# Kernel tuning notes

Hardware: AMD Instinct MI355X
Metric: run time of the kernel (lower is better)

The kernel has to match this reference:

```python
import jax, jax.numpy as jnp
import numpy as np

K = 20          # neighbors per point (knn includes the point itself, as in PyG knn)
EPS = 1e-5      # BatchNorm eps (eval mode, running stats)


def _lrelu(x):
    return jax.nn.leaky_relu(x, 0.2)


def _bn(x, g, beta, mu, var):
    # eval-mode BatchNorm1d over last (feature) axis
    return (x - mu) * (g * jax.lax.rsqrt(var + EPS)) + beta


def _edge_conv(x, W, g, beta, mu, var):
    # x: [B, N, F]. Dynamic kNN graph per batch element, edge feature [x_i, x_j - x_i],
    # Linear(no bias) -> BN -> LeakyReLU(0.2), max-aggregate over neighbors.
    sq = jnp.sum(x * x, axis=-1)                                   # [B, N]
    d2 = sq[:, :, None] + sq[:, None, :] - 2.0 * jnp.einsum('bnf,bmf->bnm', x, x)
    _, idx = jax.lax.top_k(-d2, K)                                 # [B, N, K] (self is nearest)
    xj = jax.vmap(lambda xb, ib: xb[ib])(x, idx)                   # [B, N, K, F]
    xi = jnp.broadcast_to(x[:, :, None, :], xj.shape)
    e = jnp.concatenate([xi, xj - xi], axis=-1) @ W                # [B, N, K, out]
    return jnp.max(_lrelu(_bn(e, g, beta, mu, var)), axis=2)       # [B, N, out]


def setup_inputs() -> dict:
    key = jax.random.key(0)
    ks = iter(jax.random.split(key, 64))
    B, N = 8, 2048
    d = {"pos": jax.random.normal(next(ks), (B, N, 3), jnp.float32)}

    def bn_params(name, dim):
        d["g" + name] = 0.5 + jax.random.uniform(next(ks), (dim,), jnp.float32)
        d["beta" + name] = 0.1 * jax.random.normal(next(ks), (dim,), jnp.float32)
        d["mu" + name] = 0.1 * jax.random.normal(next(ks), (dim,), jnp.float32)
        d["var" + name] = 0.5 + jax.random.uniform(next(ks), (dim,), jnp.float32)

    def lin(name, din, dout):
        d["W" + name] = jax.random.normal(next(ks), (din, dout), jnp.float32) / np.sqrt(din).astype(np.float32)

    lin("1", 2 * 3, 64);    bn_params("1", 64)
    lin("2", 2 * 64, 64);   bn_params("2", 64)
    lin("3", 2 * 64, 128);  bn_params("3", 128)
    lin("4", 2 * 128, 256); bn_params("4", 256)
    lin("m", 512, 1024);    bn_params("m", 1024)
    lin("a", 2048, 512);    bn_params("a", 512)
    lin("b", 512, 256);     bn_params("b", 256)
    d["bias_b"] = 0.01 * jax.random.normal(next(ks), (256,), jnp.float32)
    lin("c", 256, 40)
    d["bias_c"] = 0.01 * jax.random.normal(next(ks), (40,), jnp.float32)
    return d


def reference(pos, W1, g1, beta1, mu1, var1, W2, g2, beta2, mu2, var2,
              W3, g3, beta3, mu3, var3, W4, g4, beta4, mu4, var4,
              Wm, gm, betam, mum, varm, Wa, ga, betaa, mua, vara,
              Wb, gb, betab, mub, varb, bias_b, Wc, bias_c):
    x1 = _edge_conv(pos, W1, g1, beta1, mu1, var1)   # [B, N, 64]
    x2 = _edge_conv(x1, W2, g2, beta2, mu2, var2)    # [B, N, 64]
    x3 = _edge_conv(x2, W3, g3, beta3, mu3, var3)    # [B, N, 128]
    x4 = _edge_conv(x3, W4, g4, beta4, mu4, var4)    # [B, N, 256]
    h = jnp.concatenate([x1, x2, x3, x4], axis=-1)   # [B, N, 512]
    h = _lrelu(_bn(h @ Wm, gm, betam, mum, varm))    # [B, N, 1024]
    pooled = jnp.concatenate([jnp.max(h, axis=1), jnp.mean(h, axis=1)], axis=-1)  # [B, 2048]
    h = _lrelu(_bn(pooled @ Wa, ga, betaa, mua, vara))            # [B, 512]
    h = _lrelu(_bn(h @ Wb + bias_b, gb, betab, mub, varb))        # [B, 256]
    return h @ Wc + bias_c                                        # [B, 40]
```

## Files before the change

### kernel.cpp

```cpp
#include <hip/hip_runtime.h>
#include <cstdint>
#include <cstddef>

#define NPTS 2048
#define BATCH 8
#define KNN 20
#define BIGF 3.402823466e38f

typedef short bf16x8 __attribute__((ext_vector_type(8)));
typedef float f32x4 __attribute__((ext_vector_type(4)));

__device__ __forceinline__ unsigned short f2bf(float v) {
    uint32_t u = __float_as_uint(v);
    uint32_t r = (u + 0x7FFFu + ((u >> 16) & 1u)) >> 16;
    return (unsigned short)r;
}
__device__ __forceinline__ float bf2f(unsigned short h) {
    return __uint_as_float(((uint32_t)h) << 16);
}
__device__ __forceinline__ uint32_t flipkey(float d) {
    uint32_t u = __float_as_uint(d);
    return (u & 0x80000000u) ? ~u : (u | 0x80000000u);
}
__device__ __forceinline__ uint32_t d2key(float acc, float si, float sj) {
    return flipkey(fmaf(-2.f, acc, si + sj));
}
__device__ __forceinline__ uint64_t shfl_xor_u64(uint64_t v, int m) {
    int lo = __shfl_xor((int)(uint32_t)v, m, 64);
    int hi = __shfl_xor((int)(uint32_t)(v >> 32), m, 64);
    return ((uint64_t)(uint32_t)hi << 32) | (uint32_t)lo;
}

__global__ __launch_bounds__(256) void sq_kernel(const float* __restrict__ x, int lda, int F,
                                                 float* __restrict__ sq)
{
    int p = blockIdx.x * 256 + threadIdx.x;
    const float* xp = x + (size_t)p * lda;
    float s = 0.f;
    for (int f = 0; f < F; ++f) { float v = xp[f]; s = fmaf(v, v, s); }
    sq[p] = s;
}

__global__ __launch_bounds__(256) void distk_kernel(const float* __restrict__ x, int lda,
                                                    const float* __restrict__ sq,
                                                    unsigned short* __restrict__ d2u16,
                                                    int F, int b0)
{
    __shared__ __align__(16) float As[8][132];
    __shared__ __align__(16) float Bs[8][132];
    const int b  = b0 + blockIdx.z;
    const int i0 = blockIdx.x * 128;
    const int j0 = blockIdx.y * 128;
    const float* xb  = x + (size_t)b * NPTS * lda;
    const float* sqb = sq + (size_t)b * NPTS;
    const int t  = threadIdx.x;
    const int tx = t & 15, ty = t >> 4;
    const int lrow = t >> 1, lkq = (t & 1) * 4;

    float acc[8][8];
#pragma unroll
    for (int r = 0; r < 8; ++r)
#pragma unroll
        for (int c = 0; c < 8; ++c) acc[r][c] = 0.f;

    for (int k0 = 0; k0 < F; k0 += 8) {
        const float* sa = xb + (size_t)(i0 + lrow) * lda + k0 + lkq;
        const float* sb = xb + (size_t)(j0 + lrow) * lda + k0 + lkq;
        if (k0 + 8 <= F) {
            float4 a4 = *reinterpret_cast<const float4*>(sa);
            float4 b4 = *reinterpret_cast<const float4*>(sb);
            As[lkq + 0][lrow] = a4.x; As[lkq + 1][lrow] = a4.y;
            As[lkq + 2][lrow] = a4.z; As[lkq + 3][lrow] = a4.w;
            Bs[lkq + 0][lrow] = b4.x; Bs[lkq + 1][lrow] = b4.y;
            Bs[lkq + 2][lrow] = b4.z; Bs[lkq + 3][lrow] = b4.w;
        } else {
#pragma unroll
            for (int q = 0; q < 4; ++q) {
                int kk = k0 + lkq + q;
                As[lkq + q][lrow] = (kk < F) ? sa[q] : 0.f;
                Bs[lkq + q][lrow] = (kk < F) ? sb[q] : 0.f;
            }
        }
        __syncthreads();
#pragma unroll
        for (int k = 0; k < 8; ++k) {
            float4 a0 = *reinterpret_cast<const float4*>(&As[k][ty * 4]);
            float4 a1 = *reinterpret_cast<const float4*>(&As[k][64 + ty * 4]);
            float4 c0 = *reinterpret_cast<const float4*>(&Bs[k][tx * 4]);
            float4 c1 = *reinterpret_cast<const float4*>(&Bs[k][64 + tx * 4]);
            float av[8] = {a0.x, a0.y, a0.z, a0.w, a1.x, a1.y, a1.z, a1.w};
            float bv[8] = {c0.x, c0.y, c0.z, c0.w, c1.x, c1.y, c1.z, c1.w};
#pragma unroll
            for (int r = 0; r < 8; ++r)
#pragma unroll
                for (int c = 0; c < 8; ++c) acc[r][c] = fmaf(av[r], bv[c], acc[r][c]);
        }
        __syncthreads();
    }

    unsigned short* db = d2u16 + (size_t)blockIdx.z * NPTS * NPTS;
#pragma unroll
    for (int r = 0; r < 8; ++r) {
        int i = i0 + ((r < 4) ? (ty * 4 + r) : (64 + ty * 4 + r - 4));
        float si = sqb[i];
#pragma unroll
        for (int cq = 0; cq < 2; ++cq) {
            int j = j0 + (cq ? 64 : 0) + tx * 4;
            ushort4 o;
            o.x = (unsigned short)(d2key(acc[r][cq * 4 + 0], si, sqb[j + 0]) >> 16);
            o.y = (unsigned short)(d2key(acc[r][cq * 4 + 1], si, sqb[j + 1]) >> 16);
            o.z = (unsigned short)(d2key(acc[r][cq * 4 + 2], si, sqb[j + 2]) >> 16);
            o.w = (unsigned short)(d2key(acc[r][cq * 4 + 3], si, sqb[j + 3]) >> 16);
            *reinterpret_cast<ushort4*>(&db[(size_t)i * NPTS + j]) = o;
        }
    }
}

template <int F>
__global__ __launch_bounds__(256) void select_kernel(const unsigned short* __restrict__ d2u16,
                                                     const float* __restrict__ x, int lda,
                                                     const float* __restrict__ sq,
                                                     int* __restrict__ idx, int b0)
{
    const int t    = threadIdx.x;
    const int lane = t & 63;
    const int wid  = t >> 6;
    const int row_id = blockIdx.x * 4 + wid;
    const int bz = row_id >> 11;
    const int i  = row_id & 2047;
    const unsigned short* row = d2u16 + ((size_t)bz * NPTS + i) * NPTS;

    uint32_t cand[32];
#pragma unroll
    for (int s = 0; s < 4; ++s) {
        uint4 kv = *reinterpret_cast<const uint4*>(&row[s * 512 + lane * 8]);
        uint32_t cb = (uint32_t)(s * 512 + lane * 8);
        cand[s * 8 + 0] = ((kv.x & 0xFFFFu) << 16) | (cb + 0);
        cand[s * 8 + 1] = (kv.x & 0xFFFF0000u)      | (cb + 1);
        cand[s * 8 + 2] = ((kv.y & 0xFFFFu) << 16) | (cb + 2);
        cand[s * 8 + 3] = (kv.y & 0xFFFF0000u)      | (cb + 3);
        cand[s * 8 + 4] = ((kv.z & 0xFFFFu) << 16) | (cb + 4);
        cand[s * 8 + 5] = (kv.z & 0xFFFF0000u)      | (cb + 5);
        cand[s * 8 + 6] = ((kv.w & 0xFFFFu) << 16) | (cb + 6);
        cand[s * 8 + 7] = (kv.w & 0xFFFF0000u)      | (cb + 7);
    }

    const uint32_t MAXV = 0xFFFFFFFFu;
    uint32_t t1 = MAXV, t2 = MAXV, t3 = MAXV, t4 = MAXV;
#pragma unroll
    for (int s = 0; s < 32; ++s) {
        uint32_t c = cand[s];
        if (c < t4) {
            if (c < t2) {
                t4 = t3; t3 = t2;
                if (c < t1) { t2 = t1; t1 = c; } else t2 = c;
            } else {
                if (c < t3) { t4 = t3; t3 = c; } else t4 = c;
            }
        }
    }

    uint32_t keep = 0, last = 0;
    for (int it = 0; it < KNN; ++it) {
        uint32_t w = t1;
#pragma unroll
        for (int o = 1; o < 64; o <<= 1)
            w = min(w, (uint32_t)__shfl_xor((int)w, o, 64));
        keep = (lane == it) ? w : keep;
        last = w;
        if (t1 == w) {
            t1 = t2; t2 = t3; t3 = t4; t4 = MAXV;
            if (t1 == MAXV) {
#pragma unroll
                for (int s = 0; s < 32; ++s) {
                    uint32_t c = cand[s];
                    if (c > w && c < t4) {
                        if (c < t2) {
                            t4 = t3; t3 = t2;
                            if (c < t1) { t2 = t1; t1 = c; } else t2 = c;
                        } else {
                            if (c < t3) { t4 = t3; t3 = c; } else t4 = c;
                        }
                    }
                }
            }
        }
    }

    int* out = idx + ((size_t)(b0 + bz) * NPTS + i) * KNN;
    const uint32_t thr16 = last >> 16;

    int cnt = 0;
#pragma unroll
    for (int s = 0; s < 32; ++s) cnt += ((cand[s] >> 16) == thr16) ? 1 : 0;
#pragma unroll
    for (int o = 1; o < 64; o <<= 1) cnt += __shfl_xor(cnt, o, 64);

    unsigned long long bm = __ballot(lane < KNN && (keep >> 16) < thr16);
    const int sel_lt = (int)__popcll(bm);
    const int m = KNN - sel_lt;
    const bool fast = (cnt == m);

    if (lane < KNN && (fast || (keep >> 16) < thr16))
        out[lane] = (int)(keep & 0xFFFFu);
    if (fast) return;

    const float* xb  = x + (size_t)(b0 + bz) * NPTS * lda;
    const float* sqb = sq + (size_t)(b0 + bz) * NPTS;
    const float si = sqb[i];
    const float* xi = xb + (size_t)i * lda;

    uint64_t tc[4]; int ntc = 0; bool ovf = false;
#pragma unroll
    for (int s = 0; s < 32; ++s) {
        if ((cand[s] >> 16) == thr16) {
            if (ntc < 4) {
                int j = (int)(cand[s] & 0xFFFFu);
                const float* xj = xb + (size_t)j * lda;
                float dot = 0.f;
#pragma unroll
                for (int k = 0; k < F; ++k) dot = fmaf(xi[k], xj[k], dot);
                uint32_t fk = d2key(dot, si, sqb[j]);
                tc[ntc++] = ((uint64_t)fk << 32) | (uint32_t)j;
            } else ovf = true;
        }
    }
    if (__ballot(ovf)) {
        uint64_t last_ex = 0;
        for (int q = 0; q < m; ++q) {
            uint64_t lm = ~0ull;
            for (int s = 0; s < 32; ++s) {
                if ((cand[s] >> 16) == thr16) {
                    int j = (int)(cand[s] & 0xFFFFu);
                    const float* xj = xb + (size_t)j * lda;
                    float dot = 0.f;
                    for (int k = 0; k < F; ++k) dot = fmaf(xi[k], xj[k], dot);
                    uint64_t e = ((uint64_t)d2key(dot, si, sqb[j]) << 32) | (uint32_t)j;
                    if (e > last_ex && e < lm) lm = e;
                }
            }
#pragma unroll
            for (int o = 1; o < 64; o <<= 1) {
                uint64_t ov = shfl_xor_u64(lm, o);
                lm = (ov < lm) ? ov : lm;
            }
            if (lane == 0) out[sel_lt + q] = (int)(lm & 0xFFFFu);
            last_ex = lm;
        }
        return;
    }
    uint64_t last_ex = 0;
    for (int q = 0; q < m; ++q) {
        uint64_t lm = ~0ull;
#pragma unroll
        for (int u = 0; u < 4; ++u)
            if (u < ntc && tc[u] > last_ex && tc[u] < lm) lm = tc[u];
#pragma unroll
        for (int o = 1; o < 64; o <<= 1) {
            uint64_t ov = shfl_xor_u64(lm, o);
            lm = (ov < lm) ? ov : lm;
        }
        if (lane == 0) out[sel_lt + q] = (int)(lm & 0xFFFFu);
        last_ex = lm;
    }
}

__global__ __launch_bounds__(256) void gemm64_kernel(const float* __restrict__ A, int lda, int F,
                                                     const float* __restrict__ Wfull, int Fout,
                                                     float* __restrict__ apart,
                                                     float* __restrict__ bpart)
{
    __shared__ float As[16][68];
    __shared__ float Bs[16][65];
    const int i0 = blockIdx.x * 64, j0 = blockIdx.y * 64;
    const int half = blockIdx.z;
    const float* Bw = Wfull + (size_t)(half ? F : 0) * Fout;
    float* C = half ? bpart : apart;
    const int t = threadIdx.x, tx = t & 15, ty = t >> 4;
    float acc[4][4];
#pragma unroll
    for (int r = 0; r < 4; ++r)
#pragma unroll
        for (int c = 0; c < 4; ++c) acc[r][c] = 0.f;
    const int arow = t >> 2, akq = (t & 3) * 4;
    const int bk = t >> 4, bj = (t & 15) * 4;
    for (int k0 = 0; k0 < F; k0 += 16) {
#pragma unroll
        for (int q = 0; q < 4; ++q) {
            int kk = k0 + akq + q;
            As[akq + q][arow] = (kk < F) ? A[(size_t)(i0 + arow) * lda + kk] : 0.f;
        }
        {
            int kk = k0 + bk;
#pragma unroll
            for (int q = 0; q < 4; ++q)
                Bs[bk][bj + q] = (kk < F) ? Bw[(size_t)kk * Fout + j0 + bj + q] : 0.f;
        }
        __syncthreads();
#pragma unroll
        for (int k = 0; k < 16; ++k) {
            float a[4], bb[4];
#pragma unroll
            for (int r = 0; r < 4; ++r) a[r] = As[k][ty * 4 + r];
#pragma unroll
            for (int c = 0; c < 4; ++c) bb[c] = Bs[k][tx * 4 + c];
#pragma unroll
            for (int r = 0; r < 4; ++r)
#pragma unroll
                for (int c = 0; c < 4; ++c) acc[r][c] = fmaf(a[r], bb[c], acc[r][c]);
        }
        __syncthreads();
    }
#pragma unroll
    for (int r = 0; r < 4; ++r)
#pragma unroll
        for (int c = 0; c < 4; ++c)
            C[(size_t)(i0 + ty * 4 + r) * Fout + j0 + tx * 4 + c] = acc[r][c];
}

template <int FOUT>
__global__ __launch_bounds__(256) void aggregate_kernel(const float* __restrict__ apart,
                                                        const float* __restrict__ bpart,
                                                        const int* __restrict__ idx,
                                                        const float* __restrict__ g,
                                                        const float* __restrict__ be,
                                                        const float* __restrict__ mu,
                                                        const float* __restrict__ var,
                                                        float* __restrict__ out)
{
    constexpr int G   = FOUT / 4;
    constexpr int PPB = 256 / G;
    const int t  = threadIdx.x;
    const int pi = t / G;
    const int fi = t % G;
    const int p  = blockIdx.x * PPB + pi;
    const int b  = p >> 11;
    const int* nb = idx + (size_t)p * KNN;
    const float4* bp4 = reinterpret_cast<const float4*>(bpart);
    const float4* bb  = bp4 + ((size_t)b << 11) * G;

    float4 m = {-BIGF, -BIGF, -BIGF, -BIGF};
#pragma unroll 4
    for (int k = 0; k < KNN; ++k) {
        int j = nb[k];
        float4 v = bb[(size_t)j * G + fi];
        m.x = fmaxf(m.x, v.x); m.y = fmaxf(m.y, v.y);
        m.z = fmaxf(m.z, v.z); m.w = fmaxf(m.w, v.w);
    }
    float4 av = reinterpret_cast<const float4*>(apart)[(size_t)p * G + fi];
    float4 bv = bp4[(size_t)p * G + fi];
    float4 gg = reinterpret_cast<const float4*>(g)[fi];
    float4 bee = reinterpret_cast<const float4*>(be)[fi];
    float4 muu = reinterpret_cast<const float4*>(mu)[fi];
    float4 vaa = reinterpret_cast<const float4*>(var)[fi];

    float4 r;
    {
        float s, sh, vv, y;
        s = gg.x * rsqrtf(vaa.x + 1e-5f); sh = bee.x - muu.x * s;
        vv = av.x - bv.x + m.x; y = vv * s + sh; r.x = (y >= 0.f) ? y : 0.2f * y;
        s = gg.y * rsqrtf(vaa.y + 1e-5f); sh = bee.y - muu.y * s;
        vv = av.y - bv.y + m.y; y = vv * s + sh; r.y = (y >= 0.f) ? y : 0.2f * y;
        s = gg.z * rsqrtf(vaa.z + 1e-5f); sh = bee.z - muu.z * s;
        vv = av.z - bv.z + m.z; y = vv * s + sh; r.z = (y >= 0.f) ? y : 0.2f * y;
        s = gg.w * rsqrtf(vaa.w + 1e-5f); sh = bee.w - muu.w * s;
        vv = av.w - bv.w + m.w; y = vv * s + sh; r.w = (y >= 0.f) ? y : 0.2f * y;
    }
    *reinterpret_cast<float4*>(out + (size_t)p * 512 + fi * 4) = r;
}

__global__ __launch_bounds__(256) void cvt_kernel(const float* __restrict__ in,
                                                  unsigned short* __restrict__ hi,
                                                  unsigned short* __restrict__ lo)
{
    int i = blockIdx.x * 256 + threadIdx.x;
    const float4* p = reinterpret_cast<const float4*>(in) + (size_t)i * 2;
    float4 a = p[0], b = p[1];
    float v[8] = {a.x, a.y, a.z, a.w, b.x, b.y, b.z, b.w};
    uint32_t h[8], l[8];
#pragma unroll
    for (int q = 0; q < 8; ++q) {
        unsigned short hb = f2bf(v[q]);
        h[q] = hb;
        l[q] = f2bf(v[q] - bf2f(hb));
    }
    uint4 uh, ul;
    uh.x = h[0] | (h[1] << 16); uh.y = h[2] | (h[3] << 16);
    uh.z = h[4] | (h[5] << 16); uh.w = h[6] | (h[7] << 16);
    ul.x = l[0] | (l[1] << 16); ul.y = l[2] | (l[3] << 16);
    ul.z = l[4] | (l[5] << 16); ul.w = l[6] | (l[7] << 16);
    reinterpret_cast<uint4*>(hi)[i] = uh;
    reinterpret_cast<uint4*>(lo)[i] = ul;
}

__global__ __launch_bounds__(256) void cvtT_kernel(const float* __restrict__ Wm,
                                                   unsigned short* __restrict__ hiT,
                                                   unsigned short* __restrict__ loT)
{
    __shared__ float tile[32][33];
    const int n0 = blockIdx.x * 32;
    const int k0 = blockIdx.y * 32;
    const int t = threadIdx.x;
    const int c = t & 31, r = t >> 5;
#pragma unroll
    for (int rr = 0; rr < 4; ++rr)
        tile[r + rr * 8][c] = Wm[(size_t)(k0 + r + rr * 8) * 1024 + n0 + c];
    __syncthreads();
#pragma unroll
    for (int rr = 0; rr < 4; ++rr) {
        int nn = r + rr * 8, kk = c;
        float v = tile[kk][nn];
        unsigned short hb = f2bf(v);
        hiT[(size_t)(n0 + nn) * 512 + k0 + kk] = hb;
        loT[(size_t)(n0 + nn) * 512 + k0 + kk] = f2bf(v - bf2f(hb));
    }
}

__global__ __launch_bounds__(256) void wm_mfma_pool(const unsigned short* __restrict__ AH,
                                                    const unsigned short* __restrict__ AL,
                                                    const unsigned short* __restrict__ BH,
                                                    const unsigned short* __restrict__ BL,
                                                    const float* __restrict__ g,
                                                    const float* __restrict__ be,
                                                    const float* __restrict__ mu,
                                                    const float* __restrict__ var,
                                                    float* __restrict__ partmax,
                                                    float* __restrict__ partsum)
{
    __shared__ unsigned short AsH[128][40], AsL[128][40], BsH[128][40], BsL[128][40];
    __shared__ float redm[4][64], reds[4][64];
    const int t = threadIdx.x;
    const int i0 = blockIdx.x * 128, j0 = blockIdx.y * 128;
    const int lane = t & 63, wid = t >> 6, wy = wid >> 1, wx = wid & 1;
    const int lc = lane & 15, kg = lane >> 4;

    f32x4 acc[4][4];
#pragma unroll
    for (int mi = 0; mi < 4; ++mi)
#pragma unroll
        for (int ni = 0; ni < 4; ++ni) acc[mi][ni] = (f32x4){0.f, 0.f, 0.f, 0.f};

    for (int k0 = 0; k0 < 512; k0 += 32) {
        __syncthreads();
#pragma unroll
        for (int q = 0; q < 2; ++q) {
            int c = t + q * 256;
            int row = c >> 2, ko = (c & 3) * 8;
            *reinterpret_cast<uint4*>(&AsH[row][ko]) =
                *reinterpret_cast<const uint4*>(&AH[(size_t)(i0 + row) * 512 + k0 + ko]);
            *reinterpret_cast<uint4*>(&AsL[row][ko]) =
                *reinterpret_cast<const uint4*>(&AL[(size_t)(i0 + row) * 512 + k0 + ko]);
            *reinterpret_cast<uint4*>(&BsH[row][ko]) =
                *reinterpret_cast<const uint4*>(&BH[(size_t)(j0 + row) * 512 + k0 + ko]);
            *reinterpret_cast<uint4*>(&BsL[row][ko]) =
                *reinterpret_cast<const uint4*>(&BL[(size_t)(j0 + row) * 512 + k0 + ko]);
        }
        __syncthreads();

        bf16x8 aH[4], aL[4], bH[4], bL[4];
#pragma unroll
        for (int mi = 0; mi < 4; ++mi) {
            int ar = wy * 64 + mi * 16 + lc;
            aH[mi] = *reinterpret_cast<const bf16x8*>(&AsH[ar][kg * 8]);
            aL[mi] = *reinterpret_cast<const bf16x8*>(&AsL[ar][kg * 8]);
        }
#pragma unroll
        for (int ni = 0; ni < 4; ++ni) {
            int br = wx * 64 + ni * 16 + lc;
            bH[ni] = *reinterpret_cast<const bf16x8*>(&BsH[br][kg * 8]);
            bL[ni] = *reinterpret_cast<const bf16x8*>(&BsL[br][kg * 8]);
        }
#pragma unroll
        for (int mi = 0; mi < 4; ++mi)
#pragma unroll
            for (int ni = 0; ni < 4; ++ni) {
                acc[mi][ni] = __builtin_amdgcn_mfma_f32_16x16x32_bf16(aH[mi], bH[ni], acc[mi][ni], 0, 0, 0);
                acc[mi][ni] = __builtin_amdgcn_mfma_f32_16x16x32_bf16(aH[mi], bL[ni], acc[mi][ni], 0, 0, 0);
                acc[mi][ni] = __builtin_amdgcn_mfma_f32_16x16x32_bf16(aL[mi], bH[ni], acc[mi][ni], 0, 0, 0);
            }
    }

    float pmax[4], psum[4];
#pragma unroll
    for (int ni = 0; ni < 4; ++ni) {
        int j = j0 + wx * 64 + ni * 16 + lc;
        float s = g[j] * rsqrtf(var[j] + 1e-5f);
        float sh = be[j] - mu[j] * s;
        float pm = -BIGF, ps = 0.f;
#pragma unroll
        for (int mi = 0; mi < 4; ++mi)
#pragma unroll
            for (int r = 0; r < 4; ++r) {
                float y = fmaf(acc[mi][ni][r], s, sh);
                y = (y >= 0.f) ? y : 0.2f * y;
                pm = fmaxf(pm, y);
                ps += y;
            }
        pmax[ni] = pm; psum[ni] = ps;
    }
#pragma unroll
    for (int ni = 0; ni < 4; ++ni) {
        pmax[ni] = fmaxf(pmax[ni], __shfl_xor(pmax[ni], 16, 64));
        pmax[ni] = fmaxf(pmax[ni], __shfl_xor(pmax[ni], 32, 64));
        psum[ni] += __shfl_xor(psum[ni], 16, 64);
        psum[ni] += __shfl_xor(psum[ni], 32, 64);
    }
    if (lane < 16) {
#pragma unroll
        for (int ni = 0; ni < 4; ++ni) {
            redm[wid][ni * 16 + lc] = pmax[ni];
            reds[wid][ni * 16 + lc] = psum[ni];
        }
    }
    __syncthreads();
    if (t < 128) {
        int wxq = t >> 6, cl = t & 63;
        float m = fmaxf(redm[wxq][cl], redm[2 + wxq][cl]);
        float sv = reds[wxq][cl] + reds[2 + wxq][cl];
        int b = i0 >> 11, rb = (i0 & 2047) >> 7;
        partmax[((size_t)b * 16 + rb) * 1024 + j0 + t] = m;
        partsum[((size_t)b * 16 + rb) * 1024 + j0 + t] = sv;
    }
}

__global__ __launch_bounds__(256) void pool2_kernel(const float* __restrict__ partmax,
                                                    const float* __restrict__ partsum,
                                                    float* __restrict__ pooled)
{
    const int c = blockIdx.x * 256 + threadIdx.x;
    const int b = blockIdx.y;
    float m = -BIGF, s = 0.f;
    for (int rb = 0; rb < 16; ++rb) {
        m = fmaxf(m, partmax[((size_t)b * 16 + rb) * 1024 + c]);
        s += partsum[((size_t)b * 16 + rb) * 1024 + c];
    }
    pooled[(size_t)b * 2048 + c] = m;
    pooled[(size_t)b * 2048 + 1024 + c] = s * (1.f / 2048.f);
}

__global__ __launch_bounds__(512) void fc1_partial(const float* __restrict__ pooled,
                                                   const float* __restrict__ Wa,
                                                   float* __restrict__ part)
{
    const int kk = blockIdx.x, b = blockIdx.y, c = threadIdx.x;
    __shared__ float sp[128];
    if (c < 128) sp[c] = pooled[(size_t)b * 2048 + kk * 128 + c];
    __syncthreads();
    const float* w = Wa + (size_t)kk * 128 * 512 + c;
    float acc = 0.f;
#pragma unroll 8
    for (int j = 0; j < 128; ++j) acc = fmaf(sp[j], w[(size_t)j * 512], acc);
    part[((size_t)b * 16 + kk) * 512 + c] = acc;
}

__global__ __launch_bounds__(512) void fc1_reduce(const float* __restrict__ part,
                                                  const float* __restrict__ g, const float* __restrict__ be,
                                                  const float* __restrict__ mu, const float* __restrict__ var,
                                                  float* __restrict__ t1)
{
    const int b = blockIdx.x, c = threadIdx.x;
    float acc = 0.f;
#pragma unroll
    for (int kk = 0; kk < 16; ++kk) acc += part[((size_t)b * 16 + kk) * 512 + c];
    float s = g[c] * rsqrtf(var[c] + 1e-5f);
    float y = acc * s + (be[c] - mu[c] * s);
    t1[(size_t)b * 512 + c] = (y >= 0.f) ? y : 0.2f * y;
}

__global__ __launch_bounds__(256) void fc2_partial(const float* __restrict__ t1,
                                                   const float* __restrict__ Wb,
                                                   float* __restrict__ part)
{
    const int kk = blockIdx.x, b = blockIdx.y, c = threadIdx.x;
    __shared__ float sp[128];
    if (c < 128) sp[c] = t1[(size_t)b * 512 + kk * 128 + c];
    __syncthreads();
    const float* w = Wb + (size_t)kk * 128 * 256 + c;
    float acc = 0.f;
#pragma unroll 8
    for (int j = 0; j < 128; ++j) acc = fmaf(sp[j], w[(size_t)j * 256], acc);
    part[((size_t)b * 4 + kk) * 256 + c] = acc;
}

__global__ __launch_bounds__(256) void fc2_reduce(const float* __restrict__ part,
                                                  const float* __restrict__ bias_b,
                                                  const float* __restrict__ g, const float* __restrict__ be,
                                                  const float* __restrict__ mu, const float* __restrict__ var,
                                                  float* __restrict__ t2)
{
    const int b = blockIdx.x, c = threadIdx.x;
    float acc = bias_b[c];
#pragma unroll
    for (int kk = 0; kk < 4; ++kk) acc += part[((size_t)b * 4 + kk) * 256 + c];
    float s = g[c] * rsqrtf(var[c] + 1e-5f);
    float y = acc * s + (be[c] - mu[c] * s);
    t2[(size_t)b * 256 + c] = (y >= 0.f) ? y : 0.2f * y;
}

__global__ __launch_bounds__(64) void fc3_kernel(const float* __restrict__ t2,
                                                 const float* __restrict__ Wc,
                                                 const float* __restrict__ bias_c,
                                                 float* __restrict__ out)
{
    const int b = blockIdx.x, c = threadIdx.x;
    __shared__ float sp[256];
    for (int k = c; k < 256; k += 64) sp[k] = t2[(size_t)b * 256 + k];
    __syncthreads();
    if (c < 40) {
        float acc = 0.f;
#pragma unroll 8
        for (int k = 0; k < 256; ++k) acc = fmaf(sp[k], Wc[(size_t)k * 40 + c], acc);
        out[(size_t)b * 40 + c] = acc + bias_c[c];
    }
}

extern "C" void kernel_launch(void* const* d_in, const int* in_sizes, int n_in,
                              void* d_out, int out_size, void* d_ws, size_t ws_size,
                              hipStream_t stream)
{
    const float* pos = (const float*)d_in[0];
    const float* W1 = (const float*)d_in[1];
    const float* g1 = (const float*)d_in[2];  const float* be1 = (const float*)d_in[3];
    const float* mu1 = (const float*)d_in[4]; const float* va1 = (const float*)d_in[5];
    const float* W2 = (const float*)d_in[6];
    const float* g2 = (const float*)d_in[7];  const float* be2 = (const float*)d_in[8];
    const float* mu2 = (const float*)d_in[9]; const float* va2 = (const float*)d_in[10];
    const float* W3 = (const float*)d_in[11];
    const float* g3 = (const float*)d_in[12]; const float* be3 = (const float*)d_in[13];
    const float* mu3 = (const float*)d_in[14];const float* va3 = (const float*)d_in[15];
    const float* W4 = (const float*)d_in[16];
    const float* g4 = (const float*)d_in[17]; const float* be4 = (const float*)d_in[18];
    const float* mu4 = (const float*)d_in[19];const float* va4 = (const float*)d_in[20];
    const float* Wm = (const float*)d_in[21];
    const float* gm = (const float*)d_in[22]; const float* bem = (const float*)d_in[23];
    const float* mum = (const float*)d_in[24];const float* vam = (const float*)d_in[25];
    const float* Wa = (const float*)d_in[26];
    const float* ga = (const float*)d_in[27]; const float* bea = (const float*)d_in[28];
    const float* mua = (const float*)d_in[29];const float* vaa = (const float*)d_in[30];
    const float* Wb = (const float*)d_in[31];
    const float* gb = (const float*)d_in[32]; const float* beb = (const float*)d_in[33];
    const float* mub = (const float*)d_in[34];const float* vab = (const float*)d_in[35];
    const float* bias_b = (const float*)d_in[36];
    const float* Wc = (const float*)d_in[37];
    const float* bias_c = (const float*)d_in[38];

    char* ws = (char*)d_ws;
    size_t off = 0;
    auto alloc = [&](size_t bytes) -> void* {
        void* p = ws + off;
        off += (bytes + 255) & ~(size_t)255;
        return p;
    };
    float* xcat    = (float*)alloc((size_t)16384 * 512 * 4);
    float* sq      = (float*)alloc((size_t)16384 * 4);
    int*   idx     = (int*)  alloc((size_t)16384 * KNN * 4);
    float* apart   = (float*)alloc((size_t)16384 * 256 * 4);
    float* bpart   = (float*)alloc((size_t)16384 * 256 * 4);
    float* partmax = (float*)alloc((size_t)8 * 16 * 1024 * 4);
    float* partsum = (float*)alloc((size_t)8 * 16 * 1024 * 4);
    float* pooled  = (float*)alloc((size_t)8 * 2048 * 4);
    float* t1      = (float*)alloc((size_t)8 * 512 * 4);
    float* t2      = (float*)alloc((size_t)8 * 256 * 4);
    float* part1   = (float*)alloc((size_t)8 * 16 * 512 * 4);
    float* part2   = (float*)alloc((size_t)8 * 4 * 256 * 4);
    unsigned short* ah   = (unsigned short*)alloc((size_t)16384 * 512 * 2);
    unsigned short* al   = (unsigned short*)alloc((size_t)16384 * 512 * 2);
    unsigned short* wmtH = (unsigned short*)alloc((size_t)1024 * 512 * 2);
    unsigned short* wmtL = (unsigned short*)alloc((size_t)1024 * 512 * 2);
    const size_t fixed = off;
    const size_t per_b16 = (size_t)NPTS * NPTS * 2;

    int CB; unsigned short* d2u16;
    if      (ws_size >= fixed + 8 * per_b16) { CB = 8; d2u16 = (unsigned short*)(ws + fixed); }
    else if (ws_size >= fixed + 4 * per_b16) { CB = 4; d2u16 = (unsigned short*)(ws + fixed); }
    else { CB = 4; d2u16 = (unsigned short*)apart; }

    struct LayerDesc {
        const float* xin; int lda; int F; int Fout;
        float* xout; const float* W;
        const float* g; const float* be; const float* mu; const float* va;
    };
    LayerDesc Ls[4] = {
        { pos,        3,   3,   64,  xcat + 0,   W1, g1, be1, mu1, va1 },
        { xcat + 0,   512, 64,  64,  xcat + 64,  W2, g2, be2, mu2, va2 },
        { xcat + 64,  512, 64,  128, xcat + 128, W3, g3, be3, mu3, va3 },
        { xcat + 128, 512, 128, 256, xcat + 256, W4, g4, be4, mu4, va4 },
    };

    for (int L = 0; L < 4; ++L) {
        const LayerDesc& ld = Ls[L];
        sq_kernel<<<64, 256, 0, stream>>>(ld.xin, ld.lda, ld.F, sq);
        for (int b0 = 0; b0 < BATCH; b0 += CB) {
            int cb = (BATCH - b0 < CB) ? (BATCH - b0) : CB;
            distk_kernel<<<dim3(16, 16, cb), 256, 0, stream>>>(ld.xin, ld.lda, sq, d2u16, ld.F, b0);
            if (ld.F == 3)
                select_kernel<3><<<512 * cb, 256, 0, stream>>>(d2u16, ld.xin, ld.lda, sq, idx, b0);
            else if (ld.F == 64)
                select_kernel<64><<<512 * cb, 256, 0, stream>>>(d2u16, ld.xin, ld.lda, sq, idx, b0);
            else
                select_kernel<128><<<512 * cb, 256, 0, stream>>>(d2u16, ld.xin, ld.lda, sq, idx, b0);
        }
        gemm64_kernel<<<dim3(256, ld.Fout / 64, 2), 256, 0, stream>>>(
            ld.xin, ld.lda, ld.F, ld.W, ld.Fout, apart, bpart);
        if (ld.Fout == 64)
            aggregate_kernel<64><<<1024, 256, 0, stream>>>(apart, bpart, idx,
                ld.g, ld.be, ld.mu, ld.va, ld.xout);
        else if (ld.Fout == 128)
            aggregate_kernel<128><<<2048, 256, 0, stream>>>(apart, bpart, idx,
                ld.g, ld.be, ld.mu, ld.va, ld.xout);
        else
            aggregate_kernel<256><<<4096, 256, 0, stream>>>(apart, bpart, idx,
                ld.g, ld.be, ld.mu, ld.va, ld.xout);
    }

    cvt_kernel<<<4096, 256, 0, stream>>>(xcat, ah, al);
    cvtT_kernel<<<dim3(32, 16), 256, 0, stream>>>(Wm, wmtH, wmtL);
    wm_mfma_pool<<<dim3(128, 8), 256, 0, stream>>>(ah, al, wmtH, wmtL,
                                                   gm, bem, mum, vam, partmax, partsum);
    pool2_kernel<<<dim3(4, 8), 256, 0, stream>>>(partmax, partsum, pooled);
    fc1_partial<<<dim3(16, 8), 512, 0, stream>>>(pooled, Wa, part1);
    fc1_reduce<<<8, 512, 0, stream>>>(part1, ga, bea, mua, vaa, t1);
    fc2_partial<<<dim3(4, 8), 256, 0, stream>>>(t1, Wb, part2);
    fc2_reduce<<<8, 256, 0, stream>>>(part2, bias_b, gb, beb, mub, vab, t2);
    fc3_kernel<<<8, 64, 0, stream>>>(t2, Wc, bias_c, (float*)d_out);
}
```

Baseline: 856.7 us.

## Exploit distance-matrix symmetry: compute upper-triangle tiles and mirror via LDS transpose

The pairwise distance kernel now launches only the 136 upper-triangular 128x128 tiles per batch instead of all 256. Each off-diagonal tile writes its own quantized keys, stages them in shared memory, and writes the transposed tile to the mirrored location. This roughly halves the GEMM work for the kNN distance stage. In exchange it adds shared-memory traffic, an extra barrier, a serial tile-index decode loop, and narrower (ushort2) transposed stores. Mirrored values are bitwise identical, whereas the old code computed d(j,i) separately, so tie-breaking could change slightly.

```diff
diff --git a/kernel.cpp b/kernel.cpp
--- a/kernel.cpp
+++ b/kernel.cpp
@@ -41,16 +41,23 @@
     sq[p] = s;
 }
 
-__global__ __launch_bounds__(256) void distk_kernel(const float* __restrict__ x, int lda,
-                                                    const float* __restrict__ sq,
-                                                    unsigned short* __restrict__ d2u16,
-                                                    int F, int b0)
+__global__ __launch_bounds__(256) void distk_sym(const float* __restrict__ x, int lda,
+                                                 const float* __restrict__ sq,
+                                                 unsigned short* __restrict__ d2u16,
+                                                 int F, int b0)
 {
     __shared__ __align__(16) float As[8][132];
     __shared__ __align__(16) float Bs[8][132];
-    const int b  = b0 + blockIdx.z;
-    const int i0 = blockIdx.x * 128;
-    const int j0 = blockIdx.y * 128;
+    __shared__ unsigned short tb[128][130];
+
+    int tid = blockIdx.x;
+    int ti = 0;
+    while (tid >= 16 - ti) { tid -= 16 - ti; ++ti; }
+    const int tj = ti + tid;
+    const int i0 = ti * 128;
+    const int j0 = tj * 128;
+
+    const int b  = b0 + blockIdx.y;
     const float* xb  = x + (size_t)b * NPTS * lda;
     const float* sqb = sq + (size_t)b * NPTS;
     const int t  = threadIdx.x;
@@ -98,20 +105,39 @@
         __syncthreads();
     }
 
-    unsigned short* db = d2u16 + (size_t)blockIdx.z * NPTS * NPTS;
+    unsigned short* db = d2u16 + (size_t)blockIdx.y * NPTS * NPTS;
+    const bool mirror = (ti != tj);
 #pragma unroll
     for (int r = 0; r < 8; ++r) {
-        int i = i0 + ((r < 4) ? (ty * 4 + r) : (64 + ty * 4 + r - 4));
+        int il = (r < 4) ? (ty * 4 + r) : (64 + ty * 4 + r - 4);
+        int i = i0 + il;
         float si = sqb[i];
 #pragma unroll
         for (int cq = 0; cq < 2; ++cq) {
-            int j = j0 + (cq ? 64 : 0) + tx * 4;
+            int jl = (cq ? 64 : 0) + tx * 4;
+            int j = j0 + jl;
             ushort4 o;
             o.x = (unsigned short)(d2key(acc[r][cq * 4 + 0], si, sqb[j + 0]) >> 16);
             o.y = (unsigned short)(d2key(acc[r][cq * 4 + 1], si, sqb[j + 1]) >> 16);
             o.z = (unsigned short)(d2key(acc[r][cq * 4 + 2], si, sqb[j + 2]) >> 16);
             o.w = (unsigned short)(d2key(acc[r][cq * 4 + 3], si, sqb[j + 3]) >> 16);
             *reinterpret_cast<ushort4*>(&db[(size_t)i * NPTS + j]) = o;
+            if (mirror) {
+                ushort2 p0; p0.x = o.x; p0.y = o.y;
+                ushort2 p1; p1.x = o.z; p1.y = o.w;
+                *reinterpret_cast<ushort2*>(&tb[il][jl])     = p0;
+                *reinterpret_cast<ushort2*>(&tb[il][jl + 2]) = p1;
+            }
+        }
+    }
+    if (mirror) {
+        __syncthreads();
+        const int lane = t & 63, w = t >> 6;
+        for (int jj = w; jj < 128; jj += 4) {
+            ushort2 v;
+            v.x = tb[2 * lane + 0][jj];
+            v.y = tb[2 * lane + 1][jj];
+            *reinterpret_cast<ushort2*>(&db[(size_t)(j0 + jj) * NPTS + i0 + 2 * lane]) = v;
         }
     }
 }
@@ -692,7 +718,7 @@
         sq_kernel<<<64, 256, 0, stream>>>(ld.xin, ld.lda, ld.F, sq);
         for (int b0 = 0; b0 < BATCH; b0 += CB) {
             int cb = (BATCH - b0 < CB) ? (BATCH - b0) : CB;
-            distk_kernel<<<dim3(16, 16, cb), 256, 0, stream>>>(ld.xin, ld.lda, sq, d2u16, ld.F, b0);
+            distk_sym<<<dim3(136, cb), 256, 0, stream>>>(ld.xin, ld.lda, sq, d2u16, ld.F, b0);
             if (ld.F == 3)
                 select_kernel<3><<<512 * cb, 256, 0, stream>>>(d2u16, ld.xin, ld.lda, sq, idx, b0);
             else if (ld.F == 64)
```

New measurement: 802.8 us. 6.3% less time.
